# Performance work log

Measured on AMD Instinct MI355X. Metric: run time of the kernel, lower is better.

## Reference

```python
import jax, jax.numpy as jnp
import numpy as np

B, S, V, E, H = 256, 64, 30000, 300, 512
D_A, R, C, P = 350, 8, 150, 16
NUM_ITERS = 3
EPS = 1e-9


def _xavier(k, shape, fi, fo):
    lim = (6.0 / (fi + fo)) ** 0.5
    return jax.random.uniform(k, shape, minval=-lim, maxval=lim, dtype=jnp.float32)


def setup_inputs() -> dict:
    key = jax.random.key(0)
    ks = jax.random.split(key, 14)
    u = 1.0 / (H ** 0.5)
    uni = lambda k, shp: jax.random.uniform(k, shp, minval=-u, maxval=u, dtype=jnp.float32)
    return {
        'input_x': jax.random.randint(ks[0], (B, S), 0, V, dtype=jnp.int32),
        'lens': jnp.full((B,), S, dtype=jnp.int32),
        'embedding': jax.random.normal(ks[1], (V, E), dtype=jnp.float32) * 0.1,
        'w_ih_f': uni(ks[2], (4 * H, E)), 'w_hh_f': uni(ks[3], (4 * H, H)),
        'b_ih_f': uni(ks[4], (4 * H,)), 'b_hh_f': uni(ks[5], (4 * H,)),
        'w_ih_b': uni(ks[6], (4 * H, E)), 'w_hh_b': uni(ks[7], (4 * H, H)),
        'b_ih_b': uni(ks[8], (4 * H,)), 'b_hh_b': uni(ks[9], (4 * H,)),
        'ws1': _xavier(ks[10], (D_A, 2 * H), 2 * H, D_A),
        'ws2': _xavier(ks[11], (R, D_A), D_A, R),
        'capsule_weights': _xavier(ks[12], (R, 2 * H, C * P), 2 * H, C * P),
    }


def _lstm_dir(x, w_ih, w_hh, b_ih, b_hh, reverse):
    # x: [S, B, E] -> hidden states [S, B, H] (torch gate order i, f, g, o)
    b = x.shape[1]
    def step(carry, xt):
        h, c = carry
        z = xt @ w_ih.T + h @ w_hh.T + (b_ih + b_hh)
        i, f, g, o = jnp.split(z, 4, axis=-1)
        c = jax.nn.sigmoid(f) * c + jax.nn.sigmoid(i) * jnp.tanh(g)
        h = jax.nn.sigmoid(o) * jnp.tanh(c)
        return (h, c), h
    init = (jnp.zeros((b, H), x.dtype), jnp.zeros((b, H), x.dtype))
    _, hs = jax.lax.scan(step, init, x, reverse=reverse)
    return hs


def _squash(s):
    # tool.squash: (|s|^2 / (1+|s|^2)) * s / |s|
    n2 = jnp.sum(s * s, axis=-1, keepdims=True)
    return (n2 / (1.0 + n2)) * s / jnp.sqrt(n2 + EPS)


def _forward(input_x, embedding, w_ih_f, w_hh_f, b_ih_f, b_hh_f,
             w_ih_b, w_hh_b, b_ih_b, b_hh_b, ws1, ws2, capsule_weights):
    # embed; torch transposes [B,S] -> [S,B] then embeds -> [S,B,E]
    emb = embedding[input_x.T]
    # bidirectional LSTM (lens == S, so pack/pad is identity)
    h_fwd = _lstm_dir(emb, w_ih_f, w_hh_f, b_ih_f, b_hh_f, reverse=False)
    h_bwd = _lstm_dir(emb, w_ih_b, w_hh_b, b_ih_b, b_hh_b, reverse=True)
    output = jnp.transpose(jnp.concatenate([h_fwd, h_bwd], axis=-1), (1, 0, 2))  # [B,S,2H]
    # structured self-attention (dropout is identity at p=0 / eval)
    pre = jnp.tanh(jnp.einsum('bsd,ad->bsa', output, ws1))          # [B,S,d_a]
    att = jnp.einsum('bsa,ra->brs', pre, ws2)                        # [B,r,S]
    attention = jax.nn.softmax(att, axis=-1)
    semantic = jnp.einsum('brs,bsd->brd', attention, output)         # [B,r,2H]
    # prediction vectors: sum_d semantic[b,r,d] * W[r,d,k]
    pred = jnp.einsum('brd,rdk->brk', semantic, capsule_weights)
    pred = pred.reshape(-1, R, C, P)                                 # [B,r,C,P]
    # dynamic routing
    logits = jnp.zeros((pred.shape[0], R, C), pred.dtype)
    routes = None
    v = None
    for _ in range(NUM_ITERS):
        routes = jax.nn.softmax(logits, axis=2)                      # [B,r,C]
        preact = jnp.einsum('brc,brcp->bcp', routes, pred)           # [B,C,P]
        v = _squash(preact)
        logits = logits + jnp.einsum('brcp,bcp->brc', pred, v)
    class_logits = jnp.linalg.norm(v, axis=-1)                       # [B,C]
    return attention, class_logits, pred, routes


def reference(input_x, lens, embedding, w_ih_f, w_hh_f, b_ih_f, b_hh_f,
              w_ih_b, w_hh_b, b_ih_b, b_hh_b, ws1, ws2, capsule_weights):
    del lens  # all lengths == S: pack/pad identity
    return _forward(input_x, embedding, w_ih_f, w_hh_f, b_ih_f, b_hh_f,
                    w_ih_b, w_hh_b, b_ih_b, b_hh_b, ws1, ws2, capsule_weights)
```

## Files before the change

kernel.cpp:

```cpp
#include <hip/hip_runtime.h>
#include <hip/hip_bf16.h>
#include <hip/hip_cooperative_groups.h>
#include <math.h>

#define BB 256
#define SS 64
#define EE 300
#define EPX 320
#define KP 832
#define VV 30000
#define HH 512
#define H2 1024
#define DA 350
#define RR 8
#define CC 150
#define PP 16
#define CP 2400
#define NFLAG (SS * 2 * 4)

#define ATT_OFF    0L
#define CL_OFF     131072L
#define PRED_OFF   169472L
#define ROUTES_OFF 5084672L

typedef _Float16 f16;
typedef f16  f16x8 __attribute__((ext_vector_type(8)));
typedef f16  f16x4 __attribute__((ext_vector_type(4)));
typedef float f32x4 __attribute__((ext_vector_type(4)));

static __device__ __forceinline__ float sigmJ(float x) { return 1.0f / (1.0f + expf(-x)); }

#define NG_ ((long)SS * BB * EPX)
#define NW_ ((long)2 * 2048 * KP)
#define NS_ ((long)384 * 1024)
__global__ __launch_bounds__(256) void j_stage(
    const int* __restrict__ ids, const float* __restrict__ emb,
    const float* __restrict__ wihF, const float* __restrict__ whhF,
    const float* __restrict__ wihB, const float* __restrict__ whhB,
    const float* __restrict__ ws1,
    f16* __restrict__ X16, f16* __restrict__ W16, f16* __restrict__ ws1_16,
    unsigned* __restrict__ flags)
{
    const long idx = (long)blockIdx.x * 256 + threadIdx.x;
    if (idx < NG_) {
        const int e = (int)(idx % EPX);
        const int row = (int)(idx / EPX);
        const int s = row >> 8, b = row & 255;
        int tok = ids[(long)b * SS + s];
        if ((unsigned)tok >= (unsigned)VV) tok = 0;
        X16[idx] = (e < EE) ? (f16)emb[(long)tok * EE + e] : (f16)0.0f;
    } else if (idx < NG_ + NW_) {
        const long i2 = idx - NG_;
        const int dir = (int)(i2 / (2048 * KP));
        const int rem = (int)(i2 % (2048 * KP));
        const int j = rem / KP, k = rem % KP;
        const float* wih = dir ? wihB : wihF;
        const float* whh = dir ? whhB : whhF;
        float v;
        if (k < EE)        v = wih[(long)j * EE + k];
        else if (k < EPX)  v = 0.0f;
        else               v = whh[(long)j * HH + (k - EPX)];
        W16[i2] = (f16)v;
    } else if (idx < NG_ + NW_ + NS_) {
        const long i3 = idx - NG_ - NW_;
        const int j = (int)(i3 >> 10);
        ws1_16[i3] = (j < DA) ? (f16)ws1[i3] : (f16)0.0f;
    } else if (idx < NG_ + NW_ + NS_ + NFLAG) {
        flags[idx - NG_ - NW_ - NS_] = 0u;
    }
}

__global__ __launch_bounds__(256) void j_packcapsT(
    const float* __restrict__ caps, f16* __restrict__ capsT)
{
    __shared__ float t[32][33];
    const int r = blockIdx.z, k0 = blockIdx.x * 32, n0 = blockIdx.y * 32;
    const int tx = threadIdx.x & 31, ty = threadIdx.x >> 5;
    #pragma unroll
    for (int p = 0; p < 4; ++p) {
        const int k = k0 + ty + p * 8;
        const int n = n0 + tx;
        t[ty + p * 8][tx] = (n < CP) ? caps[((long)r * H2 + k) * CP + n] : 0.0f;
    }
    __syncthreads();
    #pragma unroll
    for (int p = 0; p < 4; ++p) {
        const int n = n0 + ty + p * 8;
        if (n < 2432)
            capsT[((long)r * 2432 + n) * H2 + k0 + tx] = (f16)t[tx][ty + p * 8];
    }
}

__global__ __launch_bounds__(512, 1) void p_lstm5(
    const f16* __restrict__ X16, f16* __restrict__ hs16,
    f16* __restrict__ hx, unsigned* __restrict__ flags,
    const f16* __restrict__ W16,
    const float* __restrict__ bihF, const float* __restrict__ bhhF,
    const float* __restrict__ bihB, const float* __restrict__ bhhB)
{
    __shared__ f16 Wl[4 * 26 * 64 * 8];
    __shared__ f32x4 part[4][64][4];
    __shared__ f16 hstage[64][16];

    const int bid = blockIdx.x;
    const int dir = bid & 1;
    const int bq  = (bid >> 1) & 3;
    const int ut  = bid >> 3;
    const int u0  = ut * 16;
    const int b0  = bq * 64;
    const int tid = threadIdx.x;
    const int wave = tid >> 6, lane = tid & 63;
    const int bt = wave & 3, kh = wave >> 2;
    const int l15 = lane & 15;
    const int kgrp = (lane >> 4) * 8;

    {
        const f16* Wsrc = W16 + (long)dir * 2048 * KP;
        for (int f = tid; f < 4 * 26 * 64; f += 512) {
            const int g  = f / (26 * 64);
            const int rm = f % (26 * 64);
            const int kt = rm >> 6, ln = rm & 63;
            const long src = ((long)g * HH + u0 + (ln & 15)) * KP + kt * 32 + ((ln >> 4) * 8);
            *(f16x8*)(Wl + (long)f * 8) = *(const f16x8*)(Wsrc + src);
        }
    }
    __syncthreads();

    const int arow = b0 + bt * 16 + l15;
    const int u = u0 + l15;
    const float* bi = dir ? bihB : bihF;
    const float* bh = dir ? bhhB : bhhF;
    const float bias0 = bi[u]          + bh[u];
    const float bias1 = bi[HH + u]     + bh[HH + u];
    const float bias2 = bi[2 * HH + u] + bh[2 * HH + u];
    const float bias3 = bi[3 * HH + u] + bh[3 * HH + u];
    const int rbase = (lane >> 4) * 4;
    float cc[4] = {0.f, 0.f, 0.f, 0.f};

    f32x4 xacc[4];
    const int xb = kh ? 5 : 0;
    auto computeX = [&](int se) {
        #pragma unroll
        for (int g = 0; g < 4; ++g) xacc[g] = (f32x4){0.f, 0.f, 0.f, 0.f};
        const f16* Xrow = X16 + ((long)se * BB + arow) * EPX;
        #pragma unroll
        for (int j = 0; j < 5; ++j) {
            const int kt = xb + j;
            const int k0 = kt * 32 + kgrp;
            const f16x8 afr = *(const f16x8*)(Xrow + k0);
            #pragma unroll
            for (int g = 0; g < 4; ++g) {
                const f16x8 bfr = *(const f16x8*)(Wl + (((g * 26 + kt) << 6) + lane) * 8);
                xacc[g] = __builtin_amdgcn_mfma_f32_16x16x32_f16(afr, bfr, xacc[g], 0, 0, 0);
            }
        }
    };
    computeX(dir ? (SS - 1) : 0);

    const int hb = kh ? 8 : 0;
    for (int s = 0; s < SS; ++s) {
        const int s_eff = dir ? (SS - 1 - s) : s;

        if (s > 0) {
            if (tid == 0) {
                const int fi = ((s - 1) * 2 + dir) * 4 + bq;
                int guard = 0;
                while (__hip_atomic_load(&flags[fi], __ATOMIC_RELAXED,
                                         __HIP_MEMORY_SCOPE_AGENT) < 32u) {
                    __builtin_amdgcn_s_sleep(1);
                    if (++guard > (1 << 22)) break;
                }
            }
            __syncthreads();
        }

        f32x4 acc[4];
        #pragma unroll
        for (int g = 0; g < 4; ++g) acc[g] = xacc[g];

        if (s > 0) {
            const f16* hrow = hx + ((((long)((s - 1) & 1) * 2 + dir) * BB) + arow) * HH;
            #pragma unroll
            for (int j = 0; j < 8; ++j) {
                const int kt = 10 + hb + j;
                const int hk = (hb + j) * 32 + kgrp;
                union { unsigned long long q[2]; f16x8 v; } uu;
                const unsigned long long* hp = (const unsigned long long*)(hrow + hk);
                uu.q[0] = __hip_atomic_load(hp,     __ATOMIC_RELAXED, __HIP_MEMORY_SCOPE_AGENT);
                uu.q[1] = __hip_atomic_load(hp + 1, __ATOMIC_RELAXED, __HIP_MEMORY_SCOPE_AGENT);
                #pragma unroll
                for (int g = 0; g < 4; ++g) {
                    const f16x8 bfr = *(const f16x8*)(Wl + (((g * 26 + kt) << 6) + lane) * 8);
                    acc[g] = __builtin_amdgcn_mfma_f32_16x16x32_f16(uu.v, bfr, acc[g], 0, 0, 0);
                }
            }
        }

        if (kh == 1) {
            #pragma unroll
            for (int g = 0; g < 4; ++g) part[bt][lane][g] = acc[g];
        }
        __syncthreads();
        if (kh == 0) {
            #pragma unroll
            for (int g = 0; g < 4; ++g) acc[g] += part[bt][lane][g];
            #pragma unroll
            for (int i = 0; i < 4; ++i) {
                const int b = b0 + bt * 16 + rbase + i;
                const float zi = acc[0][i] + bias0;
                const float zf = acc[1][i] + bias1;
                const float zg = acc[2][i] + bias2;
                const float zo = acc[3][i] + bias3;
                cc[i] = sigmJ(zf) * cc[i] + sigmJ(zi) * tanhf(zg);
                const float hv = sigmJ(zo) * tanhf(cc[i]);
                hs16[((long)b * SS + s_eff) * H2 + dir * HH + u] = (f16)hv;
                hstage[bt * 16 + rbase + i][l15] = (f16)hv;
            }
        }
        __syncthreads();

        {
            f16* hxw = hx + (((long)(s & 1) * 2 + dir) * BB) * HH;
            if (tid < 256) {
                const int row = tid >> 2, ch = tid & 3;
                union { unsigned long long q; f16 h4[4]; } pk;
                pk.h4[0] = hstage[row][ch * 4 + 0];
                pk.h4[1] = hstage[row][ch * 4 + 1];
                pk.h4[2] = hstage[row][ch * 4 + 2];
                pk.h4[3] = hstage[row][ch * 4 + 3];
                __hip_atomic_store(
                    (unsigned long long*)(hxw + (long)(b0 + row) * HH + u0 + ch * 4),
                    pk.q, __ATOMIC_RELAXED, __HIP_MEMORY_SCOPE_AGENT);
            }
            asm volatile("s_waitcnt vmcnt(0)" ::: "memory");
        }
        __syncthreads();
        if (tid == 0)
            __hip_atomic_fetch_add(&flags[(s * 2 + dir) * 4 + bq], 1u,
                                   __ATOMIC_RELAXED, __HIP_MEMORY_SCOPE_AGENT);

        if (s + 1 < SS) computeX(dir ? (SS - 2 - s) : (s + 1));
    }
}

__global__ __launch_bounds__(256) void j_preG(
    const f16* __restrict__ hs16, const f16* __restrict__ ws1_16,
    f16* __restrict__ pre16)
{
    const int n0 = blockIdx.x * 192;
    const int m0 = blockIdx.y * 64;
    const int tid = threadIdx.x;
    const int wave = tid >> 6, lane = tid & 63;
    const int l15 = lane & 15;
    const int kgrp = (lane >> 4) * 8;
    const f16* Arow = hs16 + (long)(m0 + wave * 16 + l15) * H2;

    f32x4 acc[12];
    #pragma unroll
    for (int nt = 0; nt < 12; ++nt) acc[nt] = (f32x4){0.f, 0.f, 0.f, 0.f};

    for (int kt = 0; kt < 32; ++kt) {
        const int k0 = kt * 32 + kgrp;
        const f16x8 afr = *(const f16x8*)(Arow + k0);
        #pragma unroll
        for (int nt = 0; nt < 12; ++nt) {
            const f16x8 bfr = *(const f16x8*)(ws1_16 + (long)(n0 + nt * 16 + l15) * H2 + k0);
            acc[nt] = __builtin_amdgcn_mfma_f32_16x16x32_f16(afr, bfr, acc[nt], 0, 0, 0);
        }
    }

    const int rbase = (lane >> 4) * 4;
    #pragma unroll
    for (int nt = 0; nt < 12; ++nt) {
        const int n = n0 + nt * 16 + l15;
        if (n < DA) {
            #pragma unroll
            for (int i = 0; i < 4; ++i) {
                const int m = m0 + wave * 16 + rbase + i;
                pre16[(long)m * DA + n] = (f16)tanhf(acc[nt][i]);
            }
        }
    }
}

__global__ __launch_bounds__(256) void j_att(
    const f16* __restrict__ pre16, const float* __restrict__ ws2,
    float* __restrict__ att_out)
{
    __shared__ f16 preS[SS * DA];
    __shared__ float w2S[RR * DA];
    __shared__ float logS[RR * SS];
    __shared__ float rmax[RR], rsum[RR];
    const int b = blockIdx.x, tid = threadIdx.x;
    {
        const unsigned long long* src =
            (const unsigned long long*)(pre16 + (long)b * SS * DA);
        unsigned long long* dst = (unsigned long long*)preS;
        for (int i = tid; i < SS * DA / 4; i += 256) dst[i] = src[i];
    }
    for (int i = tid; i < RR * DA; i += 256) w2S[i] = ws2[i];
    __syncthreads();
    for (int pp = tid; pp < RR * SS; pp += 256) {
        const int r = pp >> 6, s = pp & 63;
        const f16* prow = &preS[s * DA];
        const float* wrow = &w2S[r * DA];
        float a = 0.0f;
        for (int k = 0; k < DA; ++k) a = fmaf((float)prow[k], wrow[k], a);
        logS[r * SS + s] = a;
    }
    __syncthreads();
    if (tid < RR) {
        float mx = -1e30f;
        for (int s = 0; s < SS; ++s) mx = fmaxf(mx, logS[tid * SS + s]);
        float sm = 0.0f;
        for (int s = 0; s < SS; ++s) sm += expf(logS[tid * SS + s] - mx);
        rmax[tid] = mx; rsum[tid] = sm;
    }
    __syncthreads();
    for (int pp = tid; pp < RR * SS; pp += 256) {
        const int r = pp >> 6;
        att_out[(long)b * RR * SS + pp] = expf(logS[pp] - rmax[r]) / rsum[r];
    }
}

__global__ __launch_bounds__(256) void j_sem(
    const float* __restrict__ att, const f16* __restrict__ hs16,
    f16* __restrict__ sem16)
{
    __shared__ float aS[RR * SS];
    const int b = blockIdx.x, tid = threadIdx.x;
    for (int i = tid; i < RR * SS; i += 256) aS[i] = att[(long)b * RR * SS + i];
    __syncthreads();
    const int d0 = tid * 4;
    float acc[RR][4] = {};
    const f16* hb = hs16 + (long)b * SS * H2;
    for (int s = 0; s < SS; ++s) {
        const f16x4 hv = *(const f16x4*)(hb + s * H2 + d0);
        const float h0 = hv[0], h1 = hv[1], h2 = hv[2], h3 = hv[3];
        #pragma unroll
        for (int r = 0; r < RR; ++r) {
            const float a = aS[r * SS + s];
            acc[r][0] = fmaf(a, h0, acc[r][0]);
            acc[r][1] = fmaf(a, h1, acc[r][1]);
            acc[r][2] = fmaf(a, h2, acc[r][2]);
            acc[r][3] = fmaf(a, h3, acc[r][3]);
        }
    }
    #pragma unroll
    for (int r = 0; r < RR; ++r) {
        f16x4 o; o[0] = (f16)acc[r][0]; o[1] = (f16)acc[r][1];
        o[2] = (f16)acc[r][2]; o[3] = (f16)acc[r][3];
        *(f16x4*)(sem16 + ((long)b * RR + r) * H2 + d0) = o;
    }
}

__global__ __launch_bounds__(512) void j_predG(
    const f16* __restrict__ sem16, const f16* __restrict__ capsT16,
    float* __restrict__ pred_out)
{
    const int n0 = blockIdx.x * 64;
    const int r  = blockIdx.y;
    const int tid = threadIdx.x;
    const int wave = tid >> 6, lane = tid & 63;
    const int l15 = lane & 15;
    const int kgrp = (lane >> 4) * 8;
    const f16* Bp = capsT16 + (long)r * 2432 * H2;
    const f16* A0 = sem16 + ((long)(wave * 32 + l15) * RR + r) * H2;

    f32x4 acc[2][4];
    #pragma unroll
    for (int mt = 0; mt < 2; ++mt)
        #pragma unroll
        for (int nt = 0; nt < 4; ++nt) acc[mt][nt] = (f32x4){0.f, 0.f, 0.f, 0.f};

    for (int kt = 0; kt < 32; ++kt) {
        const int k0 = kt * 32 + kgrp;
        const f16x8 a0 = *(const f16x8*)(A0 + k0);
        const f16x8 a1 = *(const f16x8*)(A0 + (long)16 * RR * H2 + k0);
        #pragma unroll
        for (int nt = 0; nt < 4; ++nt) {
            const f16x8 bfr = *(const f16x8*)(Bp + (long)(n0 + nt * 16 + l15) * H2 + k0);
            acc[0][nt] = __builtin_amdgcn_mfma_f32_16x16x32_f16(a0, bfr, acc[0][nt], 0, 0, 0);
            acc[1][nt] = __builtin_amdgcn_mfma_f32_16x16x32_f16(a1, bfr, acc[1][nt], 0, 0, 0);
        }
    }

    const int rbase = (lane >> 4) * 4;
    #pragma unroll
    for (int mt = 0; mt < 2; ++mt) {
        #pragma unroll
        for (int nt = 0; nt < 4; ++nt) {
            const int n = n0 + nt * 16 + l15;
            if (n < CP) {
                #pragma unroll
                for (int i = 0; i < 4; ++i) {
                    const int m = wave * 32 + mt * 16 + rbase + i;
                    pred_out[((long)m * RR + r) * CP + n] = acc[mt][nt][i];
                }
            }
        }
    }
}

__global__ __launch_bounds__(256) void j_route(
    const float* __restrict__ pred,
    float* __restrict__ cls_out, float* __restrict__ routes_out)
{
    __shared__ float predS[RR * CP];
    __shared__ float logitS[RR * CC];
    __shared__ float routeS[RR * CC];
    __shared__ float preactS[CP];
    __shared__ float vS[CP];
    __shared__ float scaleS[CC];
    __shared__ float rmax[RR], rsum[RR];
    const int b = blockIdx.x, tid = threadIdx.x;
    const float* ps = pred + (long)b * RR * CP;
    for (int i = tid; i < RR * CP; i += 256) predS[i] = ps[i];
    for (int i = tid; i < RR * CC; i += 256) logitS[i] = 0.0f;
    __syncthreads();

    for (int it = 0; it < 3; ++it) {
        if (tid < RR) {
            float mx = -1e30f;
            for (int c = 0; c < CC; ++c) mx = fmaxf(mx, logitS[tid * CC + c]);
            float sm = 0.0f;
            for (int c = 0; c < CC; ++c) sm += expf(logitS[tid * CC + c] - mx);
            rmax[tid] = mx; rsum[tid] = sm;
        }
        __syncthreads();
        for (int i = tid; i < RR * CC; i += 256) {
            const int r = i / CC;
            routeS[i] = expf(logitS[i] - rmax[r]) / rsum[r];
        }
        __syncthreads();
        for (int cp = tid; cp < CP; cp += 256) {
            const int c = cp >> 4;
            float a = 0.0f;
            #pragma unroll
            for (int r = 0; r < RR; ++r)
                a = fmaf(routeS[r * CC + c], predS[r * CP + cp], a);
            preactS[cp] = a;
        }
        __syncthreads();
        for (int c = tid; c < CC; c += 256) {
            float n2 = 0.0f;
            #pragma unroll
            for (int p = 0; p < PP; ++p) { const float x = preactS[c * PP + p]; n2 = fmaf(x, x, n2); }
            scaleS[c] = (n2 / (1.0f + n2)) / sqrtf(n2 + 1e-9f);
        }
        __syncthreads();
        for (int cp = tid; cp < CP; cp += 256) vS[cp] = preactS[cp] * scaleS[cp >> 4];
        __syncthreads();
        for (int i = tid; i < RR * CC; i += 256) {
            const int r = i / CC, c = i % CC;
            float a = 0.0f;
            #pragma unroll
            for (int p = 0; p < PP; ++p)
                a = fmaf(predS[r * CP + c * PP + p], vS[c * PP + p], a);
            logitS[i] += a;
        }
        __syncthreads();
    }

    for (int i = tid; i < RR * CC; i += 256)
        routes_out[(long)b * RR * CC + i] = routeS[i];
    for (int c = tid; c < CC; c += 256) {
        float n2 = 0.0f;
        #pragma unroll
        for (int p = 0; p < PP; ++p) { const float x = vS[c * PP + p]; n2 = fmaf(x, x, n2); }
        cls_out[(long)b * CC + c] = sqrtf(n2);
    }
}

extern "C" void kernel_launch(void* const* d_in, const int* in_sizes, int n_in,
                              void* d_out, int out_size, void* d_ws, size_t ws_size,
                              hipStream_t stream)
{
    (void)in_sizes; (void)n_in; (void)out_size;
    const int*   ids   = (const int*)d_in[0];
    const float* emb   = (const float*)d_in[2];
    const float* wih_f = (const float*)d_in[3];
    const float* whh_f = (const float*)d_in[4];
    const float* bih_f = (const float*)d_in[5];
    const float* bhh_f = (const float*)d_in[6];
    const float* wih_b = (const float*)d_in[7];
    const float* whh_b = (const float*)d_in[8];
    const float* bih_b = (const float*)d_in[9];
    const float* bhh_b = (const float*)d_in[10];
    const float* ws1   = (const float*)d_in[11];
    const float* ws2   = (const float*)d_in[12];
    const float* caps  = (const float*)d_in[13];
    float* out = (float*)d_out;

    float* ws = (float*)d_ws;
    f16*  hs16   = (f16*)ws;
    f16*  hx     = (f16*)(ws + 8388608);
    f16*  X16    = (f16*)(ws + 8650752);
    f16*  W16    = (f16*)(ws + 11272192);
    f16*  ws1_16 = (f16*)(ws + 12976128);
    f16*  sem16  = (f16*)(ws + 13172736);
    unsigned* flags = (unsigned*)(ws + 14221312);
    f16*  pre16  = X16;
    f16*  capsT16 = (f16*)ws;
    const size_t need = (size_t)(14221312 + 512) * 4;
    if (ws_size < need) return;

    {
        const long total = NG_ + NW_ + NS_ + NFLAG;
        j_stage<<<(int)((total + 255) / 256), 256, 0, stream>>>(
            ids, emb, wih_f, whh_f, wih_b, whh_b, ws1, X16, W16, ws1_16, flags);
    }

    {
        const f16* a0 = X16; f16* a1 = hs16; f16* a2 = hx; unsigned* a3 = flags;
        const f16* a4 = W16;
        const float* a5 = bih_f; const float* a6 = bhh_f;
        const float* a7 = bih_b; const float* a8 = bhh_b;
        void* kargs[] = {(void*)&a0, (void*)&a1, (void*)&a2, (void*)&a3, (void*)&a4,
                         (void*)&a5, (void*)&a6, (void*)&a7, (void*)&a8};
        hipLaunchCooperativeKernel((void*)p_lstm5, dim3(256), dim3(512),
                                   kargs, 0, stream);
    }

    j_preG<<<dim3(2, 256), 256, 0, stream>>>(hs16, ws1_16, pre16);

    j_att<<<BB, 256, 0, stream>>>(pre16, ws2, out + ATT_OFF);

    j_sem<<<BB, 256, 0, stream>>>(out + ATT_OFF, hs16, sem16);

    j_packcapsT<<<dim3(32, 76, 8), 256, 0, stream>>>(caps, capsT16);

    j_predG<<<dim3(38, 8), 512, 0, stream>>>(sem16, capsT16, out + PRED_OFF);

    j_route<<<BB, 256, 0, stream>>>(out + PRED_OFF, out + CL_OFF, out + ROUTES_OFF);
}
```

Before: 834.7 us.

## Batch h loads, defer hs16 stores past flag signal, fuse att+sem, widen route

In the recurrent LSTM kernel, all eight h-tile atomic loads are issued before the MFMA loop so their latencies overlap. The hs16 history write is moved out of the gate math and done as packed 8-byte stores after the step flag is published, taking it off the critical path between timesteps. The attention and semantic kernels are fused so attention weights stay in shared memory instead of a global round trip, and the routing kernel uses 512 threads per block. Loading all h values up front raises register pressure in a kernel limited to one block per CU.

```diff
diff --git a/kernel.cpp b/kernel.cpp
--- a/kernel.cpp
+++ b/kernel.cpp
@@ -28,12 +28,12 @@
 typedef f16  f16x4 __attribute__((ext_vector_type(4)));
 typedef float f32x4 __attribute__((ext_vector_type(4)));
 
-static __device__ __forceinline__ float sigmJ(float x) { return 1.0f / (1.0f + expf(-x)); }
+static __device__ __forceinline__ float sigmM(float x) { return 1.0f / (1.0f + expf(-x)); }
 
 #define NG_ ((long)SS * BB * EPX)
 #define NW_ ((long)2 * 2048 * KP)
 #define NS_ ((long)384 * 1024)
-__global__ __launch_bounds__(256) void j_stage(
+__global__ __launch_bounds__(256) void m_stage(
     const int* __restrict__ ids, const float* __restrict__ emb,
     const float* __restrict__ wihF, const float* __restrict__ whhF,
     const float* __restrict__ wihB, const float* __restrict__ whhB,
@@ -70,7 +70,7 @@
     }
 }
 
-__global__ __launch_bounds__(256) void j_packcapsT(
+__global__ __launch_bounds__(256) void m_packcapsT(
     const float* __restrict__ caps, f16* __restrict__ capsT)
 {
     __shared__ float t[32][33];
@@ -91,7 +91,7 @@
     }
 }
 
-__global__ __launch_bounds__(512, 1) void p_lstm5(
+__global__ __launch_bounds__(512, 1) void p_lstm7(
     const f16* __restrict__ X16, f16* __restrict__ hs16,
     f16* __restrict__ hx, unsigned* __restrict__ flags,
     const f16* __restrict__ W16,
@@ -180,14 +180,19 @@
 
         if (s > 0) {
             const f16* hrow = hx + ((((long)((s - 1) & 1) * 2 + dir) * BB) + arow) * HH;
+            unsigned long long q0[8], q1[8];
+            #pragma unroll
+            for (int j = 0; j < 8; ++j) {
+                const unsigned long long* hp =
+                    (const unsigned long long*)(hrow + (hb + j) * 32 + kgrp);
+                q0[j] = __hip_atomic_load(hp,     __ATOMIC_RELAXED, __HIP_MEMORY_SCOPE_AGENT);
+                q1[j] = __hip_atomic_load(hp + 1, __ATOMIC_RELAXED, __HIP_MEMORY_SCOPE_AGENT);
+            }
             #pragma unroll
             for (int j = 0; j < 8; ++j) {
                 const int kt = 10 + hb + j;
-                const int hk = (hb + j) * 32 + kgrp;
                 union { unsigned long long q[2]; f16x8 v; } uu;
-                const unsigned long long* hp = (const unsigned long long*)(hrow + hk);
-                uu.q[0] = __hip_atomic_load(hp,     __ATOMIC_RELAXED, __HIP_MEMORY_SCOPE_AGENT);
-                uu.q[1] = __hip_atomic_load(hp + 1, __ATOMIC_RELAXED, __HIP_MEMORY_SCOPE_AGENT);
+                uu.q[0] = q0[j]; uu.q[1] = q1[j];
                 #pragma unroll
                 for (int g = 0; g < 4; ++g) {
                     const f16x8 bfr = *(const f16x8*)(Wl + (((g * 26 + kt) << 6) + lane) * 8);
@@ -206,15 +211,12 @@
             for (int g = 0; g < 4; ++g) acc[g] += part[bt][lane][g];
             #pragma unroll
             for (int i = 0; i < 4; ++i) {
-                const int b = b0 + bt * 16 + rbase + i;
                 const float zi = acc[0][i] + bias0;
                 const float zf = acc[1][i] + bias1;
                 const float zg = acc[2][i] + bias2;
                 const float zo = acc[3][i] + bias3;
-                cc[i] = sigmJ(zf) * cc[i] + sigmJ(zi) * tanhf(zg);
-                const float hv = sigmJ(zo) * tanhf(cc[i]);
-                hs16[((long)b * SS + s_eff) * H2 + dir * HH + u] = (f16)hv;
-                hstage[bt * 16 + rbase + i][l15] = (f16)hv;
+                cc[i] = sigmM(zf) * cc[i] + sigmM(zi) * tanhf(zg);
+                hstage[bt * 16 + rbase + i][l15] = (f16)(sigmM(zo) * tanhf(cc[i]));
             }
         }
         __syncthreads();
@@ -239,11 +241,22 @@
             __hip_atomic_fetch_add(&flags[(s * 2 + dir) * 4 + bq], 1u,
                                    __ATOMIC_RELAXED, __HIP_MEMORY_SCOPE_AGENT);
 
+        if (tid < 256) {
+            const int row = tid >> 2, ch = tid & 3;
+            union { unsigned long long q; f16 h4[4]; } pk;
+            pk.h4[0] = hstage[row][ch * 4 + 0];
+            pk.h4[1] = hstage[row][ch * 4 + 1];
+            pk.h4[2] = hstage[row][ch * 4 + 2];
+            pk.h4[3] = hstage[row][ch * 4 + 3];
+            *(unsigned long long*)(hs16 + ((long)(b0 + row) * SS + s_eff) * H2
+                                   + dir * HH + u0 + ch * 4) = pk.q;
+        }
+
         if (s + 1 < SS) computeX(dir ? (SS - 2 - s) : (s + 1));
     }
 }
 
-__global__ __launch_bounds__(256) void j_preG(
+__global__ __launch_bounds__(256) void m_preG(
     const f16* __restrict__ hs16, const f16* __restrict__ ws1_16,
     f16* __restrict__ pre16)
 {
@@ -283,13 +296,15 @@
     }
 }
 
-__global__ __launch_bounds__(256) void j_att(
+__global__ __launch_bounds__(256) void m_attsem(
     const f16* __restrict__ pre16, const float* __restrict__ ws2,
-    float* __restrict__ att_out)
+    const f16* __restrict__ hs16,
+    float* __restrict__ att_out, f16* __restrict__ sem16)
 {
     __shared__ f16 preS[SS * DA];
     __shared__ float w2S[RR * DA];
     __shared__ float logS[RR * SS];
+    __shared__ float aS[RR * SS];
     __shared__ float rmax[RR], rsum[RR];
     const int b = blockIdx.x, tid = threadIdx.x;
     {
@@ -319,18 +334,12 @@
     __syncthreads();
     for (int pp = tid; pp < RR * SS; pp += 256) {
         const int r = pp >> 6;
-        att_out[(long)b * RR * SS + pp] = expf(logS[pp] - rmax[r]) / rsum[r];
-    }
-}
-
-__global__ __launch_bounds__(256) void j_sem(
-    const float* __restrict__ att, const f16* __restrict__ hs16,
-    f16* __restrict__ sem16)
-{
-    __shared__ float aS[RR * SS];
-    const int b = blockIdx.x, tid = threadIdx.x;
-    for (int i = tid; i < RR * SS; i += 256) aS[i] = att[(long)b * RR * SS + i];
-    __syncthreads();
+        const float v = expf(logS[pp] - rmax[r]) / rsum[r];
+        att_out[(long)b * RR * SS + pp] = v;
+        aS[pp] = v;
+    }
+    __syncthreads();
+
     const int d0 = tid * 4;
     float acc[RR][4] = {};
     const f16* hb = hs16 + (long)b * SS * H2;
@@ -354,7 +363,7 @@
     }
 }
 
-__global__ __launch_bounds__(512) void j_predG(
+__global__ __launch_bounds__(512) void m_predG(
     const f16* __restrict__ sem16, const f16* __restrict__ capsT16,
     float* __restrict__ pred_out)
 {
@@ -402,7 +411,7 @@
     }
 }
 
-__global__ __launch_bounds__(256) void j_route(
+__global__ __launch_bounds__(512) void m_route(
     const float* __restrict__ pred,
     float* __restrict__ cls_out, float* __restrict__ routes_out)
 {
@@ -415,8 +424,8 @@
     __shared__ float rmax[RR], rsum[RR];
     const int b = blockIdx.x, tid = threadIdx.x;
     const float* ps = pred + (long)b * RR * CP;
-    for (int i = tid; i < RR * CP; i += 256) predS[i] = ps[i];
-    for (int i = tid; i < RR * CC; i += 256) logitS[i] = 0.0f;
+    for (int i = tid; i < RR * CP; i += 512) predS[i] = ps[i];
+    for (int i = tid; i < RR * CC; i += 512) logitS[i] = 0.0f;
     __syncthreads();
 
     for (int it = 0; it < 3; ++it) {
@@ -428,12 +437,12 @@
             rmax[tid] = mx; rsum[tid] = sm;
         }
         __syncthreads();
-        for (int i = tid; i < RR * CC; i += 256) {
+        for (int i = tid; i < RR * CC; i += 512) {
             const int r = i / CC;
             routeS[i] = expf(logitS[i] - rmax[r]) / rsum[r];
         }
         __syncthreads();
-        for (int cp = tid; cp < CP; cp += 256) {
+        for (int cp = tid; cp < CP; cp += 512) {
             const int c = cp >> 4;
             float a = 0.0f;
             #pragma unroll
@@ -442,16 +451,16 @@
             preactS[cp] = a;
         }
         __syncthreads();
-        for (int c = tid; c < CC; c += 256) {
+        for (int c = tid; c < CC; c += 512) {
             float n2 = 0.0f;
             #pragma unroll
             for (int p = 0; p < PP; ++p) { const float x = preactS[c * PP + p]; n2 = fmaf(x, x, n2); }
             scaleS[c] = (n2 / (1.0f + n2)) / sqrtf(n2 + 1e-9f);
         }
         __syncthreads();
-        for (int cp = tid; cp < CP; cp += 256) vS[cp] = preactS[cp] * scaleS[cp >> 4];
-        __syncthreads();
-        for (int i = tid; i < RR * CC; i += 256) {
+        for (int cp = tid; cp < CP; cp += 512) vS[cp] = preactS[cp] * scaleS[cp >> 4];
+        __syncthreads();
+        for (int i = tid; i < RR * CC; i += 512) {
             const int r = i / CC, c = i % CC;
             float a = 0.0f;
             #pragma unroll
@@ -462,9 +471,9 @@
         __syncthreads();
     }
 
-    for (int i = tid; i < RR * CC; i += 256)
+    for (int i = tid; i < RR * CC; i += 512)
         routes_out[(long)b * RR * CC + i] = routeS[i];
-    for (int c = tid; c < CC; c += 256) {
+    for (int c = tid; c < CC; c += 512) {
         float n2 = 0.0f;
         #pragma unroll
         for (int p = 0; p < PP; ++p) { const float x = vS[c * PP + p]; n2 = fmaf(x, x, n2); }
@@ -507,7 +516,7 @@
 
     {
         const long total = NG_ + NW_ + NS_ + NFLAG;
-        j_stage<<<(int)((total + 255) / 256), 256, 0, stream>>>(
+        m_stage<<<(int)((total + 255) / 256), 256, 0, stream>>>(
             ids, emb, wih_f, whh_f, wih_b, whh_b, ws1, X16, W16, ws1_16, flags);
     }
 
@@ -518,19 +527,17 @@
         const float* a7 = bih_b; const float* a8 = bhh_b;
         void* kargs[] = {(void*)&a0, (void*)&a1, (void*)&a2, (void*)&a3, (void*)&a4,
                          (void*)&a5, (void*)&a6, (void*)&a7, (void*)&a8};
-        hipLaunchCooperativeKernel((void*)p_lstm5, dim3(256), dim3(512),
+        hipLaunchCooperativeKernel((void*)p_lstm7, dim3(256), dim3(512),
                                    kargs, 0, stream);
     }
 
-    j_preG<<<dim3(2, 256), 256, 0, stream>>>(hs16, ws1_16, pre16);
-
-    j_att<<<BB, 256, 0, stream>>>(pre16, ws2, out + ATT_OFF);
-
-    j_sem<<<BB, 256, 0, stream>>>(out + ATT_OFF, hs16, sem16);
-
-    j_packcapsT<<<dim3(32, 76, 8), 256, 0, stream>>>(caps, capsT16);
-
-    j_predG<<<dim3(38, 8), 512, 0, stream>>>(sem16, capsT16, out + PRED_OFF);
-
-    j_route<<<BB, 256, 0, stream>>>(out + PRED_OFF, out + CL_OFF, out + ROUTES_OFF);
-}
+    m_preG<<<dim3(2, 256), 256, 0, stream>>>(hs16, ws1_16, pre16);
+
+    m_attsem<<<BB, 256, 0, stream>>>(pre16, ws2, hs16, out + ATT_OFF, sem16);
+
+    m_packcapsT<<<dim3(32, 76, 8), 256, 0, stream>>>(caps, capsT16);
+
+    m_predG<<<dim3(38, 8), 512, 0, stream>>>(sem16, capsT16, out + PRED_OFF);
+
+    m_route<<<BB, 512, 0, stream>>>(out + PRED_OFF, out + CL_OFF, out + ROUTES_OFF);
+}
```

Result: slower. 853.6 us (+2.3%).
